# Kernel optimization log

Measured on AMD Instinct MI355X. Metric: run time of the kernel, lower is better.

Reference implementation:

```python
import jax, jax.numpy as jnp
import numpy as np
from jax import lax

D = 33            # n_vertices
NEG_SLOPE = 0.2   # LeakyReLU slope
EPS_IN = 1e-5     # InstanceNorm eps


def _block(x, w, b, gamma, beta):
    # Conv2d(k=3, stride=2, pad=1) -> LeakyReLU(0.2) -> optional InstanceNorm2d(affine)
    y = lax.conv_general_dilated(x, w, (2, 2), [(1, 1), (1, 1)],
                                 dimension_numbers=('NCHW', 'OIHW', 'NCHW'))
    y = y + b[None, :, None, None]
    y = jnp.where(y >= 0, y, NEG_SLOPE * y)
    if gamma is not None:
        mu = jnp.mean(y, (2, 3), keepdims=True)
        var = jnp.var(y, (2, 3), keepdims=True)
        y = (y - mu) * lax.rsqrt(var + EPS_IN) * gamma[None, :, None, None] + beta[None, :, None, None]
    return y


def _backbone(lq, w1, b1, g1, be1, w2, b2, g2, be2, w3, b3, g3, be3,
              w4, b4, g4, be4, w5, b5):
    B = lq.shape[0]
    # F.interpolate(..., 256, bilinear, align_corners=False) == half-pixel linear, no antialias
    x = jax.image.resize(lq, (B, 3, 256, 256), method='linear', antialias=False)
    x = _block(x, w1, b1, g1, be1)   # [B,16,128,128]
    x = _block(x, w2, b2, g2, be2)   # [B,32,64,64]
    x = _block(x, w3, b3, g3, be3)   # [B,64,32,32]
    x = _block(x, w4, b4, g4, be4)   # [B,128,16,16]
    x = _block(x, w5, b5, None, None)  # [B,128,8,8]; Dropout is identity in eval
    # AdaptiveAvgPool2d(2) on 8x8 -> mean over 4x4 blocks
    x = x.reshape(B, 128, 2, 4, 2, 4).mean((3, 5))  # [B,128,2,2]
    return x.reshape(B, -1)  # [B,512]


def _trilerp(lut, r, g, b):
    # lut [3,D,D,D]; r,g,b [N] in [0, D-1]; align_corners=True + border padding
    i0 = jnp.clip(jnp.floor(r).astype(jnp.int32), 0, D - 2)
    j0 = jnp.clip(jnp.floor(g).astype(jnp.int32), 0, D - 2)
    k0 = jnp.clip(jnp.floor(b).astype(jnp.int32), 0, D - 2)
    fr, fg, fb = r - i0, g - j0, b - k0

    def c(di, dj, dk):
        return lut[:, i0 + di, j0 + dj, k0 + dk]  # [3,N]

    return (c(0, 0, 0) * (1 - fr) * (1 - fg) * (1 - fb)
            + c(0, 0, 1) * (1 - fr) * (1 - fg) * fb
            + c(0, 1, 0) * (1 - fr) * fg * (1 - fb)
            + c(0, 1, 1) * (1 - fr) * fg * fb
            + c(1, 0, 0) * fr * (1 - fg) * (1 - fb)
            + c(1, 0, 1) * fr * (1 - fg) * fb
            + c(1, 1, 0) * fr * fg * (1 - fb)
            + c(1, 1, 1) * fr * fg * fb)


def _ailut_transform(img, luts, vertices):
    # img [B,3,H,W] in [0,1]; luts [B,3,D,D,D]; vertices [B,3,D] sorted in [0,1]
    B, C, H, W = img.shape
    p = img.reshape(B, C, -1)  # [B,3,N]
    # per-(b,c) searchsorted(right=True)
    idx = jax.vmap(jax.vmap(lambda v, x: jnp.searchsorted(v, x, side='right')))(vertices, p)
    idx = jnp.clip(idx, 1, D - 1)
    v_lo = jnp.take_along_axis(vertices, idx - 1, axis=-1)
    v_hi = jnp.take_along_axis(vertices, idx, axis=-1)
    frac = (p - v_lo) / (v_hi - v_lo + 1e-8)
    coord = (idx - 1).astype(img.dtype) + frac        # [B,3,N] in [0, D-1]
    coord = jnp.clip(coord, 0.0, D - 1.0)             # border padding
    # torch grid layout (blue->W, green->H, red->D); LUT axes are (red, green, blue)
    sampled = jax.vmap(_trilerp)(luts, coord[:, 0], coord[:, 1], coord[:, 2])  # [B,3,N]
    return sampled.reshape(B, C, H, W)


def _forward(lq, w1, b1, g1, be1, w2, b2, g2, be2, w3, b3, g3, be3,
             w4, b4, g4, be4, w5, b5, lw, lb, bw, aw, ab):
    B = lq.shape[0]
    codes = _backbone(lq, w1, b1, g1, be1, w2, b2, g2, be2, w3, b3, g3, be3,
                      w4, b4, g4, be4, w5, b5)          # [B,512]
    # LUTGenerator
    weights = codes @ lw.T + lb                          # [B,3]
    luts = (weights @ bw.T).reshape(B, 3, D, D, D)       # [B,3,D,D,D]
    # AdaInt
    intervals = (codes @ aw.T + ab).reshape(B, 3, D - 1)
    intervals = jax.nn.softmax(intervals, axis=-1)
    vertices = jnp.pad(jnp.cumsum(intervals, axis=-1), ((0, 0), (0, 0), (1, 0)))  # [B,3,D]
    outs = jnp.clip(_ailut_transform(lq, luts, vertices), 0.0, 1.0)
    return outs, weights, vertices


def setup_inputs() -> dict:
    key = jax.random.key(0)
    ks = jax.random.split(key, 16)
    B = 4
    lq = jax.random.uniform(ks[0], (B, 3, 1024, 1024), jnp.float32)

    def cw(k, o, i):
        return jax.random.normal(k, (o, i, 3, 3), jnp.float32) * (1.0 / np.sqrt(i * 9))

    w1 = cw(ks[1], 16, 3);   b1 = jnp.zeros(16);  g1 = jnp.ones(16);  be1 = jnp.zeros(16)
    w2 = cw(ks[2], 32, 16);  b2 = jnp.zeros(32);  g2 = jnp.ones(32);  be2 = jnp.zeros(32)
    w3 = cw(ks[3], 64, 32);  b3 = jnp.zeros(64);  g3 = jnp.ones(64);  be3 = jnp.zeros(64)
    w4 = cw(ks[4], 128, 64); b4 = jnp.zeros(128); g4 = jnp.ones(128); be4 = jnp.zeros(128)
    w5 = cw(ks[5], 128, 128); b5 = jnp.zeros(128)

    lw = jax.random.normal(ks[6], (3, 512), jnp.float32) * 0.02
    lb = jnp.ones(3, jnp.float32)  # init: bias = ones
    # basis LUT bank: rank0 = identity LUT (meshgrid/(D-1), channel-flipped), others small
    grid = jnp.stack(jnp.meshgrid(jnp.arange(D), jnp.arange(D), jnp.arange(D),
                                  indexing='ij'), 0).astype(jnp.float32) / (D - 1)
    identity = grid[::-1].reshape(-1, 1)  # [3*D^3,1]
    bw = jnp.concatenate([identity,
                          jax.random.normal(ks[7], (3 * D ** 3, 2), jnp.float32) * 0.01], axis=1)
    aw = jax.random.normal(ks[8], (96, 512), jnp.float32) * 0.01
    ab = jnp.ones(96, jnp.float32)  # init: bias = ones
    return {'lq': lq, 'w1': w1, 'b1': b1, 'g1': g1, 'be1': be1,
            'w2': w2, 'b2': b2, 'g2': g2, 'be2': be2,
            'w3': w3, 'b3': b3, 'g3': g3, 'be3': be3,
            'w4': w4, 'b4': b4, 'g4': g4, 'be4': be4,
            'w5': w5, 'b5': b5, 'lw': lw, 'lb': lb, 'bw': bw, 'aw': aw, 'ab': ab}


def reference(lq, w1, b1, g1, be1, w2, b2, g2, be2, w3, b3, g3, be3,
              w4, b4, g4, be4, w5, b5, lw, lb, bw, aw, ab):
    return _forward(lq, w1, b1, g1, be1, w2, b2, g2, be2, w3, b3, g3, be3,
                    w4, b4, g4, be4, w5, b5, lw, lb, bw, aw, ab)
```

## Files before the change

kernel.cpp:

```cpp
#include <hip/hip_runtime.h>
#include <hip/hip_fp16.h>
#include <math.h>

#define LUT_D 33
#define LUT_D3 35937
#define NEG 0.2f
#define BATCH 4
#define HW_IMG 1048576

__global__ void k_resize(const float* __restrict__ lq, float* __restrict__ out) {
    int gid = blockIdx.x * 256 + threadIdx.x;
    if (gid >= BATCH * 3 * 256 * 256) return;
    int x  = gid & 255;
    int y  = (gid >> 8) & 255;
    int pc = gid >> 16;
    const float* in = lq + (size_t)pc * HW_IMG;
    const float* p0 = in + (4 * y + 1) * 1024 + (4 * x + 1);
    out[gid] = 0.25f * (p0[0] + p0[1] + p0[1024] + p0[1025]);
}

template<int IC, int OC, int OH, int OW, int NSPLIT, bool NORM_IN, bool STATS_OUT>
__global__ void __launch_bounds__(256) k_conv_t(
    const float* __restrict__ in, const float* __restrict__ nrm_in,
    const float* __restrict__ w, const float* __restrict__ bias,
    float* __restrict__ out, float* __restrict__ part) {
    constexpr int IH = OH * 2, IW = OW * 2;
    constexpr int ICB = IC / NSPLIT;
    constexpr int TROW = 20, TSZ = 17 * TROW;
    constexpr int WQ = ICB * 9 / 4;
    constexpr int NTX = OW / 8, NTY = OH / 8, NOCG = OC / 16;
    constexpr int NT = NTX * NTY;
    constexpr int PX = OH * OW;

    __shared__ float sIn[ICB * TSZ];
    __shared__ float swl[16 * ICB * 9];
    __shared__ float sNm[NORM_IN ? ICB * 2 : 1];

    int id = blockIdx.x;
    int ocg   = id % NOCG;   id /= NOCG;
    int icc_i = id % NSPLIT; id /= NSPLIT;
    int tx    = id % NTX;    id /= NTX;
    int ty    = id % NTY;    id /= NTY;
    int b     = id;
    int icc   = icc_i * ICB;

    int t    = threadIdx.x;
    int lane = t >> 6;
    int px   = t & 63;
    int py   = px >> 3, pxx = px & 7;
    int oc0  = ocg * 16 + lane * 4;

    if (IC == ICB) {
        const float4* wsrc = (const float4*)(w + (size_t)ocg * 16 * IC * 9);
        for (int i = t; i < 16 * IC * 9 / 4; i += 256) ((float4*)swl)[i] = wsrc[i];
    } else {
        for (int i = t; i < 16 * WQ; i += 256) {
            int ol = i / WQ, qi = i % WQ;
            ((float4*)swl)[ol * WQ + qi] =
                *(const float4*)(w + ((size_t)(ocg * 16 + ol) * IC + icc) * 9 + qi * 4);
        }
    }
    if (NORM_IN) {
        for (int i = t; i < ICB * 2; i += 256) sNm[i] = nrm_in[(b * IC + icc) * 2 + i];
    }
    __syncthreads();

    int iy0 = ty * 16 - 1;
    int xbase = tx * 16;
    const float* inb = in + (size_t)(b * IC + icc) * (IH * IW);
    for (int q = t; q < ICB * 17 * 4; q += 256) {
        int ic_l = q / 68;
        int r    = q % 68;
        int row  = r >> 2, quad = r & 3;
        int iy = iy0 + row;
        float4 v = {0.f, 0.f, 0.f, 0.f};
        if (iy >= 0 && iy < IH) {
            v = *(const float4*)(inb + (size_t)ic_l * (IH * IW) + (size_t)iy * IW + xbase + quad * 4);
            if (NORM_IN) {
                float sc = sNm[ic_l * 2], sh = sNm[ic_l * 2 + 1];
                v.x = v.x * sc + sh; v.y = v.y * sc + sh;
                v.z = v.z * sc + sh; v.w = v.w * sc + sh;
            }
        }
        *(float4*)(sIn + ic_l * TSZ + row * TROW + 4 + quad * 4) = v;
    }
    for (int h = t; h < ICB * 17; h += 256) {
        int ic_l = h / 17, row = h % 17;
        int iy = iy0 + row, ix = xbase - 1;
        float v = 0.f;
        if (iy >= 0 && iy < IH && ix >= 0) {
            v = inb[(size_t)ic_l * (IH * IW) + (size_t)iy * IW + ix];
            if (NORM_IN) v = v * sNm[ic_l * 2] + sNm[ic_l * 2 + 1];
        }
        sIn[ic_l * TSZ + row * TROW + 3] = v;
    }
    __syncthreads();

    float acc[4];
    #pragma unroll
    for (int j = 0; j < 4; j++) acc[j] = (NSPLIT == 1) ? bias[oc0 + j] : 0.f;

    for (int i2 = 0; i2 < ICB; i2++) {
        const float* tp = sIn + i2 * TSZ + py * 2 * TROW + pxx * 2 + 3;
        float x0 = tp[0],        x1 = tp[1],        x2 = tp[2];
        float x3 = tp[TROW],     x4 = tp[TROW + 1], x5 = tp[TROW + 2];
        float x6 = tp[2 * TROW], x7 = tp[2 * TROW + 1], x8 = tp[2 * TROW + 2];
        #pragma unroll
        for (int j = 0; j < 4; j++) {
            const float* wp = swl + ((lane * 4 + j) * ICB + i2) * 9;
            acc[j] = fmaf(x0, wp[0], acc[j]);
            acc[j] = fmaf(x1, wp[1], acc[j]);
            acc[j] = fmaf(x2, wp[2], acc[j]);
            acc[j] = fmaf(x3, wp[3], acc[j]);
            acc[j] = fmaf(x4, wp[4], acc[j]);
            acc[j] = fmaf(x5, wp[5], acc[j]);
            acc[j] = fmaf(x6, wp[6], acc[j]);
            acc[j] = fmaf(x7, wp[7], acc[j]);
            acc[j] = fmaf(x8, wp[8], acc[j]);
        }
    }

    int oy = ty * 8 + py, ox = tx * 8 + pxx;
    if (NSPLIT == 1) {
        int tile = ty * NTX + tx;
        #pragma unroll
        for (int j = 0; j < 4; j++) {
            float a = acc[j];
            a = a >= 0.f ? a : NEG * a;
            out[((size_t)(b * OC + oc0 + j) * OH + oy) * OW + ox] = a;
            if (STATS_OUT) {
                float s1 = a, s2 = a * a;
                for (int off = 32; off > 0; off >>= 1) {
                    s1 += __shfl_down(s1, off, 64);
                    s2 += __shfl_down(s2, off, 64);
                }
                if (px == 0) {
                    size_t pi = ((size_t)(b * OC + oc0 + j) * NT + tile) * 2;
                    part[pi] = s1; part[pi + 1] = s2;
                }
            }
        }
    } else {
        #pragma unroll
        for (int j = 0; j < 4; j++) {
            part[(size_t)icc_i * (BATCH * OC * PX) +
                 (size_t)(b * OC + oc0 + j) * PX + oy * OW + ox] = acc[j];
        }
    }
}

template<int NSPLIT, int OC, int PX, bool STATS>
__global__ void k_combine(const float* __restrict__ ps, const float* __restrict__ bias,
                          float* __restrict__ out, float* __restrict__ spart) {
    constexpr int TOT = BATCH * OC * PX;
    int e = blockIdx.x * 256 + threadIdx.x;
    if (e >= TOT) return;
    float s = 0.f;
    #pragma unroll
    for (int k = 0; k < NSPLIT; k++) s += ps[(size_t)k * TOT + e];
    int oc = (e / PX) % OC;
    s += bias[oc];
    s = s >= 0.f ? s : NEG * s;
    out[e] = s;
    if (STATS) {
        float s1 = s, s2 = s * s;
        for (int off = 32; off > 0; off >>= 1) {
            s1 += __shfl_down(s1, off, 64);
            s2 += __shfl_down(s2, off, 64);
        }
        if ((threadIdx.x & 63) == 0) {
            int widx = e >> 6;
            spart[widx * 2] = s1; spart[widx * 2 + 1] = s2;
        }
    }
}

template<int NT>
__global__ void k_norm(const float* __restrict__ part, const float* __restrict__ g,
                       const float* __restrict__ be, float invN, int C,
                       float* __restrict__ nrm) {
    int bc = blockIdx.x;
    int t  = threadIdx.x;
    float s1 = 0.f, s2 = 0.f;
    for (int i = t; i < NT; i += 64) {
        s1 += part[((size_t)bc * NT + i) * 2];
        s2 += part[((size_t)bc * NT + i) * 2 + 1];
    }
    #pragma unroll
    for (int off = 32; off > 0; off >>= 1) {
        s1 += __shfl_down(s1, off, 64);
        s2 += __shfl_down(s2, off, 64);
    }
    if (t == 0) {
        int c = bc % C;
        float m   = s1 * invN;
        float var = s2 * invN - m * m;
        float sc  = g[c] * rsqrtf(var + 1e-5f);
        nrm[bc * 2]     = sc;
        nrm[bc * 2 + 1] = be[c] - m * sc;
    }
}

__global__ void k_pool(const float* __restrict__ f5, float* __restrict__ codes) {
    int c = blockIdx.x * 256 + threadIdx.x;
    if (c >= 2048) return;
    int b = c >> 9;
    int rest = c & 511;
    int oc = rest >> 2, q = rest & 3;
    int py = (q >> 1) * 4, px = (q & 1) * 4;
    const float* p = f5 + ((size_t)(b * 128 + oc)) * 64;
    float s = 0.f;
    #pragma unroll
    for (int dy = 0; dy < 4; dy++)
        #pragma unroll
        for (int dx = 0; dx < 4; dx++)
            s += p[(py + dy) * 8 + px + dx];
    codes[c] = s * (1.f / 16.f);
}

__global__ void k_head(const float* __restrict__ codes, const float* __restrict__ lw,
                       const float* __restrict__ lb, const float* __restrict__ aw,
                       const float* __restrict__ ab, float* __restrict__ wt,
                       float* __restrict__ vert, float* __restrict__ out_w,
                       float* __restrict__ out_v) {
    int blk = blockIdx.x;
    int t = threadIdx.x;
    if (blk == 12) {
        if (t < 12) {
            int b = t / 3, j = t % 3;
            const float* c = codes + b * 512;
            const float* l = lw + j * 512;
            float s = lb[j];
            for (int k = 0; k < 512; k++) s += c[k] * l[k];
            wt[t] = s;
            out_w[t] = s;
        }
        return;
    }
    int b = blk / 3, ch = blk % 3;
    __shared__ float y[32];
    if (t < 32) {
        const float* c = codes + b * 512;
        const float* a = aw + (size_t)(ch * 32 + t) * 512;
        float s = ab[ch * 32 + t];
        for (int k = 0; k < 512; k++) s += c[k] * a[k];
        y[t] = s;
    }
    __syncthreads();
    if (t == 0) {
        float mx = y[0];
        for (int m = 1; m < 32; m++) mx = fmaxf(mx, y[m]);
        float e[32];
        float sum = 0.f;
        for (int m = 0; m < 32; m++) { e[m] = expf(y[m] - mx); sum += e[m]; }
        float inv = 1.f / sum;
        float cum = 0.f;
        float* vb = vert + (b * 3 + ch) * 33;
        float* ob = out_v + (b * 3 + ch) * 33;
        vb[0] = 0.f; ob[0] = 0.f;
        for (int m = 0; m < 32; m++) { cum += e[m] * inv; vb[m + 1] = cum; ob[m + 1] = cum; }
    }
}

__global__ void k_lutgen(const float* __restrict__ bw, const float* __restrict__ wt,
                         float4* __restrict__ lutp) {
    int gid = blockIdx.x * 256 + threadIdx.x;
    if (gid >= BATCH * LUT_D3) return;
    int b = gid / LUT_D3;
    int cell = gid - b * LUT_D3;
    int k = cell % LUT_D;
    int cn = (k < LUT_D - 1) ? cell + 1 : cell;
    float w0 = wt[b * 3], w1 = wt[b * 3 + 1], w2 = wt[b * 3 + 2];
    const float* r0p = bw + (size_t)(0 * LUT_D3 + cell) * 3;
    const float* g0p = bw + (size_t)(1 * LUT_D3 + cell) * 3;
    const float* b0p = bw + (size_t)(2 * LUT_D3 + cell) * 3;
    const float* r1p = bw + (size_t)(0 * LUT_D3 + cn) * 3;
    const float* g1p = bw + (size_t)(1 * LUT_D3 + cn) * 3;
    const float* b1p = bw + (size_t)(2 * LUT_D3 + cn) * 3;
    union { float4 f4; __half h[8]; } u;
    u.h[0] = __float2half_rn(r0p[0] * w0 + r0p[1] * w1 + r0p[2] * w2);
    u.h[1] = __float2half_rn(g0p[0] * w0 + g0p[1] * w1 + g0p[2] * w2);
    u.h[2] = __float2half_rn(b0p[0] * w0 + b0p[1] * w1 + b0p[2] * w2);
    u.h[3] = __float2half_rn(r1p[0] * w0 + r1p[1] * w1 + r1p[2] * w2);
    u.h[4] = __float2half_rn(g1p[0] * w0 + g1p[1] * w1 + g1p[2] * w2);
    u.h[5] = __float2half_rn(b1p[0] * w0 + b1p[1] * w1 + b1p[2] * w2);
    u.h[6] = __float2half_rn(0.f);
    u.h[7] = __float2half_rn(0.f);
    lutp[gid] = u.f4;
}

__device__ __forceinline__ void search1(const float* __restrict__ sv, int ch, float x,
                                        int& i0, float& f) {
    const float* v = sv + ch * LUT_D;
    int lo = 0, hi = LUT_D;
    while (lo < hi) { int mid = (lo + hi) >> 1; if (v[mid] <= x) lo = mid + 1; else hi = mid; }
    int idx = lo < 1 ? 1 : (lo > LUT_D - 1 ? LUT_D - 1 : lo);
    float vl = v[idx - 1], vh = v[idx];
    float fr = (x - vl) / (vh - vl + 1e-8f);
    float coord = (float)(idx - 1) + fr;
    coord = fminf(fmaxf(coord, 0.f), (float)(LUT_D - 1));
    i0 = (int)floorf(coord);
    if (i0 > LUT_D - 2) i0 = LUT_D - 2;
    f = coord - (float)i0;
}

__device__ __forceinline__ void decode_lerp(float4 e, float fb,
                                            float& rv, float& gv, float& bv) {
    union { float f; __half2 h; } u0, u1, u2;
    u0.f = e.x; u1.f = e.y; u2.f = e.z;
    float2 a = __half22float2(u0.h);
    float2 b = __half22float2(u1.h);
    float2 c = __half22float2(u2.h);
    rv = fmaf(fb, b.y - a.x, a.x);
    gv = fmaf(fb, c.x - a.y, a.y);
    bv = fmaf(fb, c.y - b.x, b.x);
}

__global__ void __launch_bounds__(256) k_transform(const float* __restrict__ lq,
                                                   const float4* __restrict__ lutp,
                                                   const float* __restrict__ vert,
                                                   float* __restrict__ out) {
    int bimg = blockIdx.x >> 10;
    int blk  = blockIdx.x & 1023;
    __shared__ float sv[3 * LUT_D];
    if (threadIdx.x < 3 * LUT_D) sv[threadIdx.x] = vert[bimg * 3 * LUT_D + threadIdx.x];
    __syncthreads();
    int p0 = blk * 1024 + threadIdx.x * 4;
    const float* lr = lq + (size_t)bimg * 3 * HW_IMG + p0;
    float4 r4 = *(const float4*)(lr);
    float4 g4 = *(const float4*)(lr + HW_IMG);
    float4 b4 = *(const float4*)(lr + 2 * HW_IMG);
    const float4* L = lutp + (size_t)bimg * LUT_D3;
    float rr[4] = {r4.x, r4.y, r4.z, r4.w};
    float gg[4] = {g4.x, g4.y, g4.z, g4.w};
    float bb[4] = {b4.x, b4.y, b4.z, b4.w};
    float ro[4], go[4], bo[4];
    #pragma unroll
    for (int i = 0; i < 4; i++) {
        int i0, j0, k0; float fr, fg, fb;
        search1(sv, 0, rr[i], i0, fr);
        search1(sv, 1, gg[i], j0, fg);
        search1(sv, 2, bb[i], k0, fb);
        int base = (i0 * LUT_D + j0) * LUT_D + k0;
        float4 e00 = L[base];
        float4 e01 = L[base + 33];
        float4 e10 = L[base + 1089];
        float4 e11 = L[base + 1122];
        float r00, g00, b00, r01, g01, b01, r10, g10, b10, r11, g11, b11;
        decode_lerp(e00, fb, r00, g00, b00);
        decode_lerp(e01, fb, r01, g01, b01);
        decode_lerp(e10, fb, r10, g10, b10);
        decode_lerp(e11, fb, r11, g11, b11);
        float w00 = (1.f - fr) * (1.f - fg), w01 = (1.f - fr) * fg;
        float w10 = fr * (1.f - fg),         w11 = fr * fg;
        float rx = r00 * w00 + r01 * w01 + r10 * w10 + r11 * w11;
        float ry = g00 * w00 + g01 * w01 + g10 * w10 + g11 * w11;
        float rz = b00 * w00 + b01 * w01 + b10 * w10 + b11 * w11;
        ro[i] = fminf(fmaxf(rx, 0.f), 1.f);
        go[i] = fminf(fmaxf(ry, 0.f), 1.f);
        bo[i] = fminf(fmaxf(rz, 0.f), 1.f);
    }
    float* op = out + (size_t)bimg * 3 * HW_IMG + p0;
    float4 o0 = {ro[0], ro[1], ro[2], ro[3]};
    float4 o1 = {go[0], go[1], go[2], go[3]};
    float4 o2 = {bo[0], bo[1], bo[2], bo[3]};
    *(float4*)(op) = o0;
    *(float4*)(op + HW_IMG) = o1;
    *(float4*)(op + 2 * HW_IMG) = o2;
}

extern "C" void kernel_launch(void* const* d_in, const int* in_sizes, int n_in,
                              void* d_out, int out_size, void* d_ws, size_t ws_size,
                              hipStream_t stream) {
    const float* lq  = (const float*)d_in[0];
    const float* w1  = (const float*)d_in[1];
    const float* b1  = (const float*)d_in[2];
    const float* g1  = (const float*)d_in[3];
    const float* be1 = (const float*)d_in[4];
    const float* w2  = (const float*)d_in[5];
    const float* b2  = (const float*)d_in[6];
    const float* g2  = (const float*)d_in[7];
    const float* be2 = (const float*)d_in[8];
    const float* w3  = (const float*)d_in[9];
    const float* b3  = (const float*)d_in[10];
    const float* g3  = (const float*)d_in[11];
    const float* be3 = (const float*)d_in[12];
    const float* w4  = (const float*)d_in[13];
    const float* b4  = (const float*)d_in[14];
    const float* g4  = (const float*)d_in[15];
    const float* be4 = (const float*)d_in[16];
    const float* w5  = (const float*)d_in[17];
    const float* b5  = (const float*)d_in[18];
    const float* lw  = (const float*)d_in[19];
    const float* lb  = (const float*)d_in[20];
    const float* bw  = (const float*)d_in[21];
    const float* aw  = (const float*)d_in[22];
    const float* ab  = (const float*)d_in[23];

    float* ws     = (float*)d_ws;
    float* r256   = ws;
    float* f1     = r256 + 786432;
    float* f2     = f1 + 1048576;
    float* f3     = f2 + 524288;
    float* f4     = f3 + 262144;
    float* f5     = f4 + 131072;
    float* codes  = f5 + 32768;
    float* wt     = codes + 2048;
    float* vert   = wt + 12;
    float* part1  = vert + 396;
    float* part2  = part1 + 32768;
    float* part3  = part2 + 16384;
    float* spart4 = part3 + 8192;
    float* norm1  = spart4 + 4096;
    float* norm2  = norm1 + 128;
    float* norm3  = norm2 + 256;
    float* norm4  = norm3 + 512;
    float* luts4  = norm4 + 1024;
    float* psplit4 = f1;
    float* psplit5 = f1 + 262144;

    float* outs  = (float*)d_out;
    float* out_w = outs + (size_t)BATCH * 3 * HW_IMG;
    float* out_v = out_w + 12;

    k_resize<<<3072, 256, 0, stream>>>(lq, r256);
    k_conv_t<3, 16, 128, 128, 1, false, true><<<1024, 256, 0, stream>>>(
        r256, nullptr, w1, b1, f1, part1);
    k_norm<256><<<64, 64, 0, stream>>>(part1, g1, be1, 1.f / 16384.f, 16, norm1);
    k_conv_t<16, 32, 64, 64, 1, true, true><<<512, 256, 0, stream>>>(
        f1, norm1, w2, b2, f2, part2);
    k_norm<64><<<128, 64, 0, stream>>>(part2, g2, be2, 1.f / 4096.f, 32, norm2);
    k_conv_t<32, 64, 32, 32, 1, true, true><<<256, 256, 0, stream>>>(
        f2, norm2, w3, b3, f3, part3);
    k_norm<16><<<256, 64, 0, stream>>>(part3, g3, be3, 1.f / 1024.f, 64, norm3);
    k_conv_t<64, 128, 16, 16, 2, true, false><<<256, 256, 0, stream>>>(
        f3, norm3, w4, b4, nullptr, psplit4);
    k_combine<2, 128, 256, true><<<512, 256, 0, stream>>>(psplit4, b4, f4, spart4);
    k_norm<4><<<512, 64, 0, stream>>>(spart4, g4, be4, 1.f / 256.f, 128, norm4);
    k_conv_t<128, 128, 8, 8, 4, true, false><<<128, 256, 0, stream>>>(
        f4, norm4, w5, b5, nullptr, psplit5);
    k_combine<4, 128, 64, false><<<128, 256, 0, stream>>>(psplit5, b5, f5, nullptr);
    k_pool<<<8, 256, 0, stream>>>(f5, codes);
    k_head<<<13, 64, 0, stream>>>(codes, lw, lb, aw, ab, wt, vert, out_w, out_v);
    k_lutgen<<<(BATCH * LUT_D3 + 255) / 256, 256, 0, stream>>>(bw, wt, (float4*)luts4);
    k_transform<<<BATCH * 1024, 256, 0, stream>>>(lq, (const float4*)luts4, vert, outs);
}
```

Before: 310.0 us.

## Replace binary search with bucket table and pre-gather per-cell LUT corners

Builds a 256-entry bucket table for each vertex curve in the head kernel. The transform now starts from the table entry and walks forward linearly instead of running a binary search. A new cellgen kernel packs the four corner entries of each LUT cell into 48 contiguous bytes, so each pixel does three adjacent float4 loads instead of four scattered ones. The transform also batches all index searches before the gathers to expose memory-level parallelism. The cost is an extra kernel and a 6 MB cell buffer placed over the workspace, and the linear walk can be long if the vertices are bunched.

```diff
diff --git a/kernel.cpp b/kernel.cpp
--- a/kernel.cpp
+++ b/kernel.cpp
@@ -221,8 +221,8 @@
 __global__ void k_head(const float* __restrict__ codes, const float* __restrict__ lw,
                        const float* __restrict__ lb, const float* __restrict__ aw,
                        const float* __restrict__ ab, float* __restrict__ wt,
-                       float* __restrict__ vert, float* __restrict__ out_w,
-                       float* __restrict__ out_v) {
+                       float* __restrict__ vert, float* __restrict__ stab,
+                       float* __restrict__ out_w, float* __restrict__ out_v) {
     int blk = blockIdx.x;
     int t = threadIdx.x;
     if (blk == 12) {
@@ -239,6 +239,7 @@
     }
     int b = blk / 3, ch = blk % 3;
     __shared__ float y[32];
+    __shared__ float vsh[33];
     if (t < 32) {
         const float* c = codes + b * 512;
         const float* a = aw + (size_t)(ch * 32 + t) * 512;
@@ -257,8 +258,20 @@
         float cum = 0.f;
         float* vb = vert + (b * 3 + ch) * 33;
         float* ob = out_v + (b * 3 + ch) * 33;
-        vb[0] = 0.f; ob[0] = 0.f;
-        for (int m = 0; m < 32; m++) { cum += e[m] * inv; vb[m + 1] = cum; ob[m + 1] = cum; }
+        vb[0] = 0.f; ob[0] = 0.f; vsh[0] = 0.f;
+        for (int m = 0; m < 32; m++) {
+            cum += e[m] * inv;
+            vb[m + 1] = cum; ob[m + 1] = cum; vsh[m + 1] = cum;
+        }
+    }
+    __syncthreads();
+    unsigned char* sb = (unsigned char*)stab + (b * 3 + ch) * 256;
+    for (int u = t; u < 256; u += 64) {
+        float lo = (float)u * (1.f / 256.f);
+        int cnt = 0;
+        #pragma unroll
+        for (int m = 0; m < 33; m++) cnt += (vsh[m] <= lo) ? 1 : 0;
+        sb[u] = (unsigned char)cnt;
     }
 }
 
@@ -289,25 +302,48 @@
     lutp[gid] = u.f4;
 }
 
-__device__ __forceinline__ void search1(const float* __restrict__ sv, int ch, float x,
-                                        int& i0, float& f) {
-    const float* v = sv + ch * LUT_D;
-    int lo = 0, hi = LUT_D;
-    while (lo < hi) { int mid = (lo + hi) >> 1; if (v[mid] <= x) lo = mid + 1; else hi = mid; }
-    int idx = lo < 1 ? 1 : (lo > LUT_D - 1 ? LUT_D - 1 : lo);
+__global__ void k_cellgen(const float4* __restrict__ lutp, float4* __restrict__ cells) {
+    int gid = blockIdx.x * 256 + threadIdx.x;
+    if (gid >= BATCH * 32768) return;
+    int b = gid >> 15;
+    int cell = gid & 32767;
+    int k0 = cell & 31, j0 = (cell >> 5) & 31, i0 = cell >> 10;
+    const float4* L = lutp + (size_t)b * LUT_D3;
+    int base = (i0 * LUT_D + j0) * LUT_D + k0;
+    float4 e00 = L[base];
+    float4 e01 = L[base + LUT_D];
+    float4 e10 = L[base + LUT_D * LUT_D];
+    float4 e11 = L[base + LUT_D * LUT_D + LUT_D];
+    float4 o0, o1, o2;
+    o0.x = e00.x; o0.y = e00.y; o0.z = e00.z;
+    o0.w = e01.x; o1.x = e01.y; o1.y = e01.z;
+    o1.z = e10.x; o1.w = e10.y; o2.x = e10.z;
+    o2.y = e11.x; o2.z = e11.y; o2.w = e11.z;
+    float4* dst = cells + (size_t)gid * 4;
+    dst[0] = o0; dst[1] = o1; dst[2] = o2;
+}
+
+__device__ __forceinline__ void searchA(const float* __restrict__ v,
+                                        const unsigned char* __restrict__ tab,
+                                        float x, int& i0, float& f) {
+    int u = (int)(x * 256.f);
+    u = u < 0 ? 0 : (u > 255 ? 255 : u);
+    int idx = tab[u];
+    while (idx < LUT_D && v[idx] <= x) idx++;
+    idx = idx < 1 ? 1 : (idx > LUT_D - 1 ? LUT_D - 1 : idx);
     float vl = v[idx - 1], vh = v[idx];
     float fr = (x - vl) / (vh - vl + 1e-8f);
     float coord = (float)(idx - 1) + fr;
     coord = fminf(fmaxf(coord, 0.f), (float)(LUT_D - 1));
-    i0 = (int)floorf(coord);
+    i0 = (int)coord;
     if (i0 > LUT_D - 2) i0 = LUT_D - 2;
     f = coord - (float)i0;
 }
 
-__device__ __forceinline__ void decode_lerp(float4 e, float fb,
-                                            float& rv, float& gv, float& bv) {
+__device__ __forceinline__ void decode_lerp3(float wa, float wb, float wc, float fb,
+                                             float& rv, float& gv, float& bv) {
     union { float f; __half2 h; } u0, u1, u2;
-    u0.f = e.x; u1.f = e.y; u2.f = e.z;
+    u0.f = wa; u1.f = wb; u2.f = wc;
     float2 a = __half22float2(u0.h);
     float2 b = __half22float2(u1.h);
     float2 c = __half22float2(u2.h);
@@ -317,40 +353,53 @@
 }
 
 __global__ void __launch_bounds__(256) k_transform(const float* __restrict__ lq,
-                                                   const float4* __restrict__ lutp,
+                                                   const float4* __restrict__ cells,
                                                    const float* __restrict__ vert,
+                                                   const unsigned char* __restrict__ stab,
                                                    float* __restrict__ out) {
     int bimg = blockIdx.x >> 10;
     int blk  = blockIdx.x & 1023;
     __shared__ float sv[3 * LUT_D];
+    __shared__ unsigned char st[768];
     if (threadIdx.x < 3 * LUT_D) sv[threadIdx.x] = vert[bimg * 3 * LUT_D + threadIdx.x];
+    if (threadIdx.x < 192)
+        ((unsigned int*)st)[threadIdx.x] = ((const unsigned int*)stab)[bimg * 192 + threadIdx.x];
     __syncthreads();
     int p0 = blk * 1024 + threadIdx.x * 4;
     const float* lr = lq + (size_t)bimg * 3 * HW_IMG + p0;
     float4 r4 = *(const float4*)(lr);
     float4 g4 = *(const float4*)(lr + HW_IMG);
     float4 b4 = *(const float4*)(lr + 2 * HW_IMG);
-    const float4* L = lutp + (size_t)bimg * LUT_D3;
     float rr[4] = {r4.x, r4.y, r4.z, r4.w};
     float gg[4] = {g4.x, g4.y, g4.z, g4.w};
     float bb[4] = {b4.x, b4.y, b4.z, b4.w};
+
+    int cidx[4];
+    float fra[4], fga[4], fba[4];
+    #pragma unroll
+    for (int i = 0; i < 4; i++) {
+        int i0, j0, k0;
+        searchA(sv,      st,       rr[i], i0, fra[i]);
+        searchA(sv + 33, st + 256, gg[i], j0, fga[i]);
+        searchA(sv + 66, st + 512, bb[i], k0, fba[i]);
+        cidx[i] = ((i0 * 32 + j0) << 5) + k0;
+    }
+    float4 c0[4], c1[4], c2[4];
+    #pragma unroll
+    for (int i = 0; i < 4; i++) {
+        const float4* p = cells + (((size_t)(bimg << 15) + cidx[i]) << 2);
+        c0[i] = p[0]; c1[i] = p[1]; c2[i] = p[2];
+    }
     float ro[4], go[4], bo[4];
     #pragma unroll
     for (int i = 0; i < 4; i++) {
-        int i0, j0, k0; float fr, fg, fb;
-        search1(sv, 0, rr[i], i0, fr);
-        search1(sv, 1, gg[i], j0, fg);
-        search1(sv, 2, bb[i], k0, fb);
-        int base = (i0 * LUT_D + j0) * LUT_D + k0;
-        float4 e00 = L[base];
-        float4 e01 = L[base + 33];
-        float4 e10 = L[base + 1089];
-        float4 e11 = L[base + 1122];
+        float fb = fba[i];
         float r00, g00, b00, r01, g01, b01, r10, g10, b10, r11, g11, b11;
-        decode_lerp(e00, fb, r00, g00, b00);
-        decode_lerp(e01, fb, r01, g01, b01);
-        decode_lerp(e10, fb, r10, g10, b10);
-        decode_lerp(e11, fb, r11, g11, b11);
+        decode_lerp3(c0[i].x, c0[i].y, c0[i].z, fb, r00, g00, b00);
+        decode_lerp3(c0[i].w, c1[i].x, c1[i].y, fb, r01, g01, b01);
+        decode_lerp3(c1[i].z, c1[i].w, c2[i].x, fb, r10, g10, b10);
+        decode_lerp3(c2[i].y, c2[i].z, c2[i].w, fb, r11, g11, b11);
+        float fr = fra[i], fg = fga[i];
         float w00 = (1.f - fr) * (1.f - fg), w01 = (1.f - fr) * fg;
         float w10 = fr * (1.f - fg),         w11 = fr * fg;
         float rx = r00 * w00 + r01 * w01 + r10 * w10 + r11 * w11;
@@ -415,9 +464,11 @@
     float* norm2  = norm1 + 128;
     float* norm3  = norm2 + 256;
     float* norm4  = norm3 + 512;
-    float* luts4  = norm4 + 1024;
+    float* stab   = norm4 + 1024;
+    float* luts4  = stab + 768;
     float* psplit4 = f1;
     float* psplit5 = f1 + 262144;
+    float* cells  = ws;
 
     float* outs  = (float*)d_out;
     float* out_w = outs + (size_t)BATCH * 3 * HW_IMG;
@@ -441,7 +492,9 @@
         f4, norm4, w5, b5, nullptr, psplit5);
     k_combine<4, 128, 64, false><<<128, 256, 0, stream>>>(psplit5, b5, f5, nullptr);
     k_pool<<<8, 256, 0, stream>>>(f5, codes);
-    k_head<<<13, 64, 0, stream>>>(codes, lw, lb, aw, ab, wt, vert, out_w, out_v);
+    k_head<<<13, 64, 0, stream>>>(codes, lw, lb, aw, ab, wt, vert, stab, out_w, out_v);
     k_lutgen<<<(BATCH * LUT_D3 + 255) / 256, 256, 0, stream>>>(bw, wt, (float4*)luts4);
-    k_transform<<<BATCH * 1024, 256, 0, stream>>>(lq, (const float4*)luts4, vert, outs);
-}
+    k_cellgen<<<512, 256, 0, stream>>>((const float4*)luts4, (float4*)cells);
+    k_transform<<<BATCH * 1024, 256, 0, stream>>>(
+        lq, (const float4*)cells, vert, (const unsigned char*)stab, outs);
+}
```

Result: faster. 291.8 us (-5.9%).
